# Optimization experiments

Hardware: AMD Instinct MI355X
Metric: run time of the kernel (lower is better)

The kernel has to match this reference:

```python
import jax, jax.numpy as jnp
import numpy as np

NUM_HEADS = 8
LOGIT_MAX = float(np.log(1.0 / 0.01))  # log(100)


def setup_inputs() -> dict:
    key = jax.random.key(0)
    kq, kk, kv, kp = jax.random.split(key, 4)
    B, n, L, C = 16, 100, 64, 256
    return {
        "query": jax.random.normal(kq, (B, n, L, C), dtype=jnp.float32),
        "key": jax.random.normal(kk, (B, n, L, C), dtype=jnp.float32),
        "value": jax.random.normal(kv, (B, n, L, C), dtype=jnp.float32),
        "position": jax.random.normal(kp, (B, NUM_HEADS, L, L), dtype=jnp.float32),
        "logit_scale": jnp.full((NUM_HEADS, 1, 1), np.log(10.0), dtype=jnp.float32),
    }


def reference(query, key, value, position, logit_scale):
    B, n, Lq, C = query.shape
    Lv = key.shape[2]
    H = NUM_HEADS
    Dh = C // H
    q = query.reshape(B, n, Lq, H, Dh)
    k = key.reshape(B, n, Lv, H, Dh)
    v = value.reshape(B, n, Lv, H, Dh)
    # [B, n, H, Lq, Lv]
    attn = jnp.einsum("bnqhd,bnkhd->bnhqk", q, k)
    scale = jnp.exp(jnp.minimum(logit_scale, LOGIT_MAX))  # (H,1,1)
    attn = attn * scale + position[:, None]  # broadcast over window dim n
    attn = jax.nn.softmax(attn, axis=-1)
    x = jnp.einsum("bnhqk,bnkhd->bnqhd", attn, v).reshape(B, n, Lq, C)
    return (x, attn)
```

## Files before the change

kernel.cpp:

```cpp
#include <hip/hip_runtime.h>


#define LOGIT_MAX_F 4.605170185988091f

__global__ __launch_bounds__(256) void tat_attn_kernel(
    const float* __restrict__ Qg, const float* __restrict__ Kg,
    const float* __restrict__ Vg, const float* __restrict__ Pg,
    const float* __restrict__ LSg,
    float* __restrict__ Xout, float* __restrict__ Aout)
{
    constexpr int L = 64, C = 256, Dh = 32, H = 8, NW = 100;
    constexpr int QK_STRIDE = 68;
    constexpr int P_STRIDE  = 68;

    __shared__ float Qt[Dh * QK_STRIDE];
    __shared__ float Kt[Dh * QK_STRIDE];
    __shared__ float Vs[L * Dh];
    __shared__ float Ps[L * P_STRIDE];

    const int blk = blockIdx.x;
    const int h  = blk & 7;
    const int bw = blk >> 3;
    const int t  = threadIdx.x;

    const float* qb = Qg + (size_t)bw * L * C + h * Dh;
    const float* kb = Kg + (size_t)bw * L * C + h * Dh;
    const float* vb = Vg + (size_t)bw * L * C + h * Dh;
    const int b = bw / NW;
    const float* pb = Pg + (size_t)(b * H + h) * L * L;
    float* xb = Xout + (size_t)bw * L * C + h * Dh;
    float* ab = Aout + ((size_t)bw * H + h) * L * L;

    const float scale = __expf(fminf(LSg[h], LOGIT_MAX_F));

    {
        const int row = t >> 3;
        const int d4  = (t & 7) << 2;
        #pragma unroll
        for (int p = 0; p < 2; ++p) {
            const int r = p * 32 + row;
            const float4 qv = *(const float4*)(qb + r * C + d4);
            const float4 kv = *(const float4*)(kb + r * C + d4);
            const float4 vv = *(const float4*)(vb + r * C + d4);
            Qt[(d4 + 0) * QK_STRIDE + r] = qv.x;
            Qt[(d4 + 1) * QK_STRIDE + r] = qv.y;
            Qt[(d4 + 2) * QK_STRIDE + r] = qv.z;
            Qt[(d4 + 3) * QK_STRIDE + r] = qv.w;
            Kt[(d4 + 0) * QK_STRIDE + r] = kv.x;
            Kt[(d4 + 1) * QK_STRIDE + r] = kv.y;
            Kt[(d4 + 2) * QK_STRIDE + r] = kv.z;
            Kt[(d4 + 3) * QK_STRIDE + r] = kv.w;
            *(float4*)(Vs + r * Dh + d4) = vv;
        }
    }
    __syncthreads();

    {
        const int tq = (t & 15) << 2;
        const int tk = (t >> 4) << 2;
        float acc[4][4];
        #pragma unroll
        for (int i = 0; i < 4; ++i)
            #pragma unroll
            for (int j = 0; j < 4; ++j) acc[i][j] = 0.0f;

        #pragma unroll 8
        for (int d = 0; d < Dh; ++d) {
            const float4 qv = *(const float4*)(Qt + d * QK_STRIDE + tq);
            const float4 kv = *(const float4*)(Kt + d * QK_STRIDE + tk);
            const float qa[4] = {qv.x, qv.y, qv.z, qv.w};
            const float ka[4] = {kv.x, kv.y, kv.z, kv.w};
            #pragma unroll
            for (int i = 0; i < 4; ++i)
                #pragma unroll
                for (int j = 0; j < 4; ++j)
                    acc[i][j] = fmaf(qa[i], ka[j], acc[i][j]);
        }
        #pragma unroll
        for (int i = 0; i < 4; ++i)
            *(float4*)(Ps + (tq + i) * P_STRIDE + tk) =
                make_float4(acc[i][0], acc[i][1], acc[i][2], acc[i][3]);
    }
    __syncthreads();

    {
        const int wv   = t >> 6;
        const int lane = t & 63;
        #pragma unroll 4
        for (int it = 0; it < 16; ++it) {
            const int qq = wv * 16 + it;
            const float l = fmaf(Ps[qq * P_STRIDE + lane], scale,
                                 pb[qq * L + lane]);
            float m = l;
            #pragma unroll
            for (int off = 32; off > 0; off >>= 1)
                m = fmaxf(m, __shfl_xor(m, off));
            const float e = __expf(l - m);
            float s = e;
            #pragma unroll
            for (int off = 32; off > 0; off >>= 1)
                s += __shfl_xor(s, off);
            const float pv = e / s;
            ab[qq * L + lane] = pv;
            Ps[qq * P_STRIDE + lane] = pv;
        }
    }
    __syncthreads();

    {
        const int td = (t & 7) << 2;
        const int q0 = (t >> 3) << 1;
        float a0[4] = {0, 0, 0, 0};
        float a1[4] = {0, 0, 0, 0};
        #pragma unroll 8
        for (int k = 0; k < L; ++k) {
            const float4 vv = *(const float4*)(Vs + k * Dh + td);
            const float p0 = Ps[q0 * P_STRIDE + k];
            const float p1 = Ps[(q0 + 1) * P_STRIDE + k];
            a0[0] = fmaf(p0, vv.x, a0[0]);
            a0[1] = fmaf(p0, vv.y, a0[1]);
            a0[2] = fmaf(p0, vv.z, a0[2]);
            a0[3] = fmaf(p0, vv.w, a0[3]);
            a1[0] = fmaf(p1, vv.x, a1[0]);
            a1[1] = fmaf(p1, vv.y, a1[1]);
            a1[2] = fmaf(p1, vv.z, a1[2]);
            a1[3] = fmaf(p1, vv.w, a1[3]);
        }
        *(float4*)(xb + q0 * C + td)       = make_float4(a0[0], a0[1], a0[2], a0[3]);
        *(float4*)(xb + (q0 + 1) * C + td) = make_float4(a1[0], a1[1], a1[2], a1[3]);
    }
}

extern "C" void kernel_launch(void* const* d_in, const int* in_sizes, int n_in,
                              void* d_out, int out_size, void* d_ws, size_t ws_size,
                              hipStream_t stream) {
    const float* q   = (const float*)d_in[0];
    const float* k   = (const float*)d_in[1];
    const float* v   = (const float*)d_in[2];
    const float* pos = (const float*)d_in[3];
    const float* ls  = (const float*)d_in[4];
    float* out = (float*)d_out;

    constexpr int B = 16, NW = 100, L = 64, C = 256, H = 8;
    float* x_out = out;
    float* a_out = out + (size_t)B * NW * L * C;

    const int blocks = B * NW * H;
    tat_attn_kernel<<<blocks, 256, 0, stream>>>(q, k, v, pos, ls, x_out, a_out);
}
```

Before: 620.0 us.

## Rewrite attention kernel with bf16 MFMA using split hi/lo precision for QK

Replaces the scalar FP32 QK^T and PV loops with MFMA 16x16x32 bf16 instructions. QK^T uses a three-term hi/lo bf16 split to keep near-fp32 accuracy, while P and V are rounded to plain bf16 for the output matmul. Softmax now runs directly on the MFMA accumulator registers, so the logits no longer round-trip through shared memory. Shared memory shrinks through bf16 storage and a smaller aliased footprint, and launch bounds request higher occupancy. The risk is reduced precision in X from bf16 P and V, and some uncoalesced scalar stores for the attention and X outputs.

Measured after the change: 540.2 us. -12.9%, faster.

```diff
diff --git a/kernel.cpp b/kernel.cpp
--- a/kernel.cpp
+++ b/kernel.cpp
@@ -1,133 +1,162 @@
 #include <hip/hip_runtime.h>
 
 
+typedef __attribute__((ext_vector_type(8))) short bf16x8;
+typedef __attribute__((ext_vector_type(4))) float f32x4;
+
 #define LOGIT_MAX_F 4.605170185988091f
 
-__global__ __launch_bounds__(256) void tat_attn_kernel(
+__device__ __forceinline__ short f2bf(float f) {
+    union { float f; unsigned u; } c; c.f = f;
+    unsigned r = c.u + 0x7FFFu + ((c.u >> 16) & 1u);
+    return (short)(r >> 16);
+}
+__device__ __forceinline__ float bf2f(short s) {
+    union { unsigned u; float f; } c; c.u = ((unsigned)(unsigned short)s) << 16;
+    return c.f;
+}
+
+#define QHI_OFF 0
+#define QLO_OFF 2560
+#define KHI_OFF 5120
+#define KLO_OFF 7680
+#define VT_OFF  10240
+#define P_OFF   0
+#define SMEM_SHORTS 12544
+
+__global__ __launch_bounds__(256, 5) void tat_attn_kernel(
     const float* __restrict__ Qg, const float* __restrict__ Kg,
     const float* __restrict__ Vg, const float* __restrict__ Pg,
     const float* __restrict__ LSg,
     float* __restrict__ Xout, float* __restrict__ Aout)
 {
-    constexpr int L = 64, C = 256, Dh = 32, H = 8, NW = 100;
-    constexpr int QK_STRIDE = 68;
-    constexpr int P_STRIDE  = 68;
-
-    __shared__ float Qt[Dh * QK_STRIDE];
-    __shared__ float Kt[Dh * QK_STRIDE];
-    __shared__ float Vs[L * Dh];
-    __shared__ float Ps[L * P_STRIDE];
+    constexpr int L = 64, C = 256, H = 8, NW = 100;
+    __shared__ short smem[SMEM_SHORTS];
 
     const int blk = blockIdx.x;
     const int h  = blk & 7;
     const int bw = blk >> 3;
     const int t  = threadIdx.x;
+    const int wave = t >> 6;
+    const int lane = t & 63;
+    const int quad = lane >> 4;
+    const int l15  = lane & 15;
 
-    const float* qb = Qg + (size_t)bw * L * C + h * Dh;
-    const float* kb = Kg + (size_t)bw * L * C + h * Dh;
-    const float* vb = Vg + (size_t)bw * L * C + h * Dh;
+    const float* qb = Qg + (size_t)bw * L * C + h * 32;
+    const float* kb = Kg + (size_t)bw * L * C + h * 32;
+    const float* vb = Vg + (size_t)bw * L * C + h * 32;
     const int b = bw / NW;
     const float* pb = Pg + (size_t)(b * H + h) * L * L;
-    float* xb = Xout + (size_t)bw * L * C + h * Dh;
+    float* xb = Xout + (size_t)bw * L * C + h * 32;
     float* ab = Aout + ((size_t)bw * H + h) * L * L;
 
     const float scale = __expf(fminf(LSg[h], LOGIT_MAX_F));
 
     {
-        const int row = t >> 3;
-        const int d4  = (t & 7) << 2;
+        const int r8 = t >> 2;
+        const int c8 = (t & 3) * 8;
+        const float4 q0 = *(const float4*)(qb + r8 * C + c8);
+        const float4 q1 = *(const float4*)(qb + r8 * C + c8 + 4);
+        const float4 k0 = *(const float4*)(kb + r8 * C + c8);
+        const float4 k1 = *(const float4*)(kb + r8 * C + c8 + 4);
+        const float qa[8] = {q0.x,q0.y,q0.z,q0.w,q1.x,q1.y,q1.z,q1.w};
+        const float ka[8] = {k0.x,k0.y,k0.z,k0.w,k1.x,k1.y,k1.z,k1.w};
+        bf16x8 qh, ql, kh, kl;
         #pragma unroll
-        for (int p = 0; p < 2; ++p) {
-            const int r = p * 32 + row;
-            const float4 qv = *(const float4*)(qb + r * C + d4);
-            const float4 kv = *(const float4*)(kb + r * C + d4);
-            const float4 vv = *(const float4*)(vb + r * C + d4);
-            Qt[(d4 + 0) * QK_STRIDE + r] = qv.x;
-            Qt[(d4 + 1) * QK_STRIDE + r] = qv.y;
-            Qt[(d4 + 2) * QK_STRIDE + r] = qv.z;
-            Qt[(d4 + 3) * QK_STRIDE + r] = qv.w;
-            Kt[(d4 + 0) * QK_STRIDE + r] = kv.x;
-            Kt[(d4 + 1) * QK_STRIDE + r] = kv.y;
-            Kt[(d4 + 2) * QK_STRIDE + r] = kv.z;
-            Kt[(d4 + 3) * QK_STRIDE + r] = kv.w;
-            *(float4*)(Vs + r * Dh + d4) = vv;
+        for (int i = 0; i < 8; ++i) {
+            const short qhi = f2bf(qa[i]);
+            qh[i] = qhi; ql[i] = f2bf(qa[i] - bf2f(qhi));
+            const short khi = f2bf(ka[i]);
+            kh[i] = khi; kl[i] = f2bf(ka[i] - bf2f(khi));
         }
+        *(bf16x8*)(smem + QHI_OFF + r8 * 40 + c8) = qh;
+        *(bf16x8*)(smem + QLO_OFF + r8 * 40 + c8) = ql;
+        *(bf16x8*)(smem + KHI_OFF + r8 * 40 + c8) = kh;
+        *(bf16x8*)(smem + KLO_OFF + r8 * 40 + c8) = kl;
+
+        const int kk = t & 63;
+        const int db = (t >> 6) * 8;
+        const float4 v0 = *(const float4*)(vb + kk * C + db);
+        const float4 v1 = *(const float4*)(vb + kk * C + db + 4);
+        const float va[8] = {v0.x,v0.y,v0.z,v0.w,v1.x,v1.y,v1.z,v1.w};
+        #pragma unroll
+        for (int i = 0; i < 8; ++i)
+            smem[VT_OFF + (db + i) * 72 + kk] = f2bf(va[i]);
     }
     __syncthreads();
 
+    f32x4 acc0 = {0,0,0,0}, acc1 = {0,0,0,0}, acc2 = {0,0,0,0}, acc3 = {0,0,0,0};
     {
-        const int tq = (t & 15) << 2;
-        const int tk = (t >> 4) << 2;
-        float acc[4][4];
+        const bf16x8 aqh = *(const bf16x8*)(smem + QHI_OFF + (16*wave + l15)*40 + quad*8);
+        const bf16x8 aql = *(const bf16x8*)(smem + QLO_OFF + (16*wave + l15)*40 + quad*8);
         #pragma unroll
-        for (int i = 0; i < 4; ++i)
-            #pragma unroll
-            for (int j = 0; j < 4; ++j) acc[i][j] = 0.0f;
+        for (int t4 = 0; t4 < 4; ++t4) {
+            const bf16x8 bkh = *(const bf16x8*)(smem + KHI_OFF + (16*t4 + l15)*40 + quad*8);
+            const bf16x8 bkl = *(const bf16x8*)(smem + KLO_OFF + (16*t4 + l15)*40 + quad*8);
+            f32x4 a = (t4==0)?acc0:(t4==1)?acc1:(t4==2)?acc2:acc3;
+            a = __builtin_amdgcn_mfma_f32_16x16x32_bf16(aqh, bkh, a, 0, 0, 0);
+            a = __builtin_amdgcn_mfma_f32_16x16x32_bf16(aqh, bkl, a, 0, 0, 0);
+            a = __builtin_amdgcn_mfma_f32_16x16x32_bf16(aql, bkh, a, 0, 0, 0);
+            if (t4==0) acc0 = a; else if (t4==1) acc1 = a; else if (t4==2) acc2 = a; else acc3 = a;
+        }
+    }
 
-        #pragma unroll 8
-        for (int d = 0; d < Dh; ++d) {
-            const float4 qv = *(const float4*)(Qt + d * QK_STRIDE + tq);
-            const float4 kv = *(const float4*)(Kt + d * QK_STRIDE + tk);
-            const float qa[4] = {qv.x, qv.y, qv.z, qv.w};
-            const float ka[4] = {kv.x, kv.y, kv.z, kv.w};
-            #pragma unroll
-            for (int i = 0; i < 4; ++i)
-                #pragma unroll
-                for (int j = 0; j < 4; ++j)
-                    acc[i][j] = fmaf(qa[i], ka[j], acc[i][j]);
-        }
+    float lg[4][4];
+    #pragma unroll
+    for (int r = 0; r < 4; ++r) {
+        const int row = 16*wave + quad*4 + r;
+        const int cb  = row * L + l15;
+        lg[0][r] = fmaf(acc0[r], scale, pb[cb + 0]);
+        lg[1][r] = fmaf(acc1[r], scale, pb[cb + 16]);
+        lg[2][r] = fmaf(acc2[r], scale, pb[cb + 32]);
+        lg[3][r] = fmaf(acc3[r], scale, pb[cb + 48]);
+    }
+
+    float p[4][4];
+    #pragma unroll
+    for (int r = 0; r < 4; ++r) {
+        float m = fmaxf(fmaxf(lg[0][r], lg[1][r]), fmaxf(lg[2][r], lg[3][r]));
         #pragma unroll
-        for (int i = 0; i < 4; ++i)
-            *(float4*)(Ps + (tq + i) * P_STRIDE + tk) =
-                make_float4(acc[i][0], acc[i][1], acc[i][2], acc[i][3]);
+        for (int off = 8; off > 0; off >>= 1) m = fmaxf(m, __shfl_xor(m, off));
+        const float e0 = __expf(lg[0][r] - m);
+        const float e1 = __expf(lg[1][r] - m);
+        const float e2 = __expf(lg[2][r] - m);
+        const float e3 = __expf(lg[3][r] - m);
+        float s = (e0 + e1) + (e2 + e3);
+        #pragma unroll
+        for (int off = 8; off > 0; off >>= 1) s += __shfl_xor(s, off);
+        const float inv = 1.0f / s;
+        p[0][r] = e0 * inv; p[1][r] = e1 * inv; p[2][r] = e2 * inv; p[3][r] = e3 * inv;
     }
+
     __syncthreads();
 
-    {
-        const int wv   = t >> 6;
-        const int lane = t & 63;
-        #pragma unroll 4
-        for (int it = 0; it < 16; ++it) {
-            const int qq = wv * 16 + it;
-            const float l = fmaf(Ps[qq * P_STRIDE + lane], scale,
-                                 pb[qq * L + lane]);
-            float m = l;
-            #pragma unroll
-            for (int off = 32; off > 0; off >>= 1)
-                m = fmaxf(m, __shfl_xor(m, off));
-            const float e = __expf(l - m);
-            float s = e;
-            #pragma unroll
-            for (int off = 32; off > 0; off >>= 1)
-                s += __shfl_xor(s, off);
-            const float pv = e / s;
-            ab[qq * L + lane] = pv;
-            Ps[qq * P_STRIDE + lane] = pv;
+    #pragma unroll
+    for (int r = 0; r < 4; ++r) {
+        const int row = 16*wave + quad*4 + r;
+        #pragma unroll
+        for (int t4 = 0; t4 < 4; ++t4) {
+            const int col = 16*t4 + l15;
+            ab[row * L + col] = p[t4][r];
+            smem[P_OFF + row * 72 + col] = f2bf(p[t4][r]);
         }
     }
-    __syncthreads();
 
-    {
-        const int td = (t & 7) << 2;
-        const int q0 = (t >> 3) << 1;
-        float a0[4] = {0, 0, 0, 0};
-        float a1[4] = {0, 0, 0, 0};
-        #pragma unroll 8
-        for (int k = 0; k < L; ++k) {
-            const float4 vv = *(const float4*)(Vs + k * Dh + td);
-            const float p0 = Ps[q0 * P_STRIDE + k];
-            const float p1 = Ps[(q0 + 1) * P_STRIDE + k];
-            a0[0] = fmaf(p0, vv.x, a0[0]);
-            a0[1] = fmaf(p0, vv.y, a0[1]);
-            a0[2] = fmaf(p0, vv.z, a0[2]);
-            a0[3] = fmaf(p0, vv.w, a0[3]);
-            a1[0] = fmaf(p1, vv.x, a1[0]);
-            a1[1] = fmaf(p1, vv.y, a1[1]);
-            a1[2] = fmaf(p1, vv.z, a1[2]);
-            a1[3] = fmaf(p1, vv.w, a1[3]);
-        }
-        *(float4*)(xb + q0 * C + td)       = make_float4(a0[0], a0[1], a0[2], a0[3]);
-        *(float4*)(xb + (q0 + 1) * C + td) = make_float4(a1[0], a1[1], a1[2], a1[3]);
+    f32x4 o0 = {0,0,0,0}, o1 = {0,0,0,0};
+    #pragma unroll
+    for (int hh = 0; hh < 2; ++hh) {
+        const bf16x8 ap = *(const bf16x8*)(smem + P_OFF + (16*wave + l15)*72 + hh*32 + quad*8);
+        const bf16x8 bv0 = *(const bf16x8*)(smem + VT_OFF + l15*72        + hh*32 + quad*8);
+        const bf16x8 bv1 = *(const bf16x8*)(smem + VT_OFF + (l15+16)*72   + hh*32 + quad*8);
+        o0 = __builtin_amdgcn_mfma_f32_16x16x32_bf16(ap, bv0, o0, 0, 0, 0);
+        o1 = __builtin_amdgcn_mfma_f32_16x16x32_bf16(ap, bv1, o1, 0, 0, 0);
+    }
+
+    #pragma unroll
+    for (int r = 0; r < 4; ++r) {
+        const int row = 16*wave + quad*4 + r;
+        xb[row * C + l15]      = o0[r];
+        xb[row * C + 16 + l15] = o1[r];
     }
 }
 
```
